# Performance work log

Measured on AMD Instinct MI355X. Metric: run time of the kernel, lower is better.

## Reference

```python
import jax, jax.numpy as jnp
import numpy as np

N_SUPPORT = 65536
N_QUERY = 65536
FEAT = 1024
EMBED = 512
WAYS = 256


def setup_inputs() -> dict:
    key = jax.random.key(0)
    k1, k2, k3, k4 = jax.random.split(key, 4)
    support_images = jax.random.normal(k1, (N_SUPPORT, FEAT), dtype=jnp.float32)
    query_images = jax.random.normal(k2, (N_QUERY, FEAT), dtype=jnp.float32)
    # deterministic labels so every one of the `ways` classes is non-empty
    labels = jnp.arange(N_SUPPORT, dtype=jnp.int32) % WAYS
    support_labels = jax.nn.one_hot(labels, WAYS, dtype=jnp.int32)  # one-hot, as in torch forward
    W = jax.random.normal(k3, (FEAT, EMBED), dtype=jnp.float32) / np.sqrt(FEAT).astype(np.float32)
    b = jax.random.normal(k4, (EMBED,), dtype=jnp.float32) * 0.01
    return {
        "support_images": support_images,
        "support_labels": support_labels,
        "query_images": query_images,
        "W": W,
        "b": b,
    }


def reference(support_images, support_labels, query_images, W, b):
    ways = support_labels.shape[1]
    labels = jnp.argmax(support_labels, axis=1)  # [N_support]

    # backbone: Linear(feat -> embed)
    z_support = support_images @ W + b  # [N_support, E]
    z_query = query_images @ W + b      # [N_query, E]

    # fused per-class mean (replaces the python loop over classes)
    sums = jax.ops.segment_sum(z_support, labels, num_segments=ways)          # [ways, E]
    counts = jax.ops.segment_sum(jnp.ones((z_support.shape[0],), z_support.dtype),
                                 labels, num_segments=ways)                   # [ways]
    z_proto = sums / counts[:, None]

    # scores = -cdist(z_query, z_proto)  (euclidean, p=2)
    q2 = jnp.sum(z_query * z_query, axis=1, keepdims=True)   # [Nq, 1]
    p2 = jnp.sum(z_proto * z_proto, axis=1)[None, :]          # [1, ways]
    d2 = q2 + p2 - 2.0 * (z_query @ z_proto.T)                # [Nq, ways]
    scores = -jnp.sqrt(jnp.maximum(d2, 0.0))

    return jax.nn.softmax(scores, axis=1)
```

## Files before the change

### kernel.cpp

```cpp
#include <hip/hip_runtime.h>
#include <stdint.h>

#define NSUP 65536
#define NQRY 65536
#define FEAT 1024
#define EMB  512
#define WAYS 256

typedef unsigned short u16;
typedef unsigned int   u32;
typedef __attribute__((ext_vector_type(8))) __bf16 bf16x8;
typedef __attribute__((ext_vector_type(4))) float  f32x4;

static __device__ __forceinline__ u16 f2bf(float f) {
    u32 u = __builtin_bit_cast(u32, f);
    u32 r = u + 0x7fffu + ((u >> 16) & 1u);
    return (u16)(r >> 16);
}

static __device__ __forceinline__ void gl_lds16(const void* g, void* l) {
    __builtin_amdgcn_global_load_lds((const __attribute__((address_space(1))) u32*)g,
                                     (__attribute__((address_space(3))) u32*)l,
                                     16, 0, 0);
}

__global__ __launch_bounds__(256) void k0_transpose(const float* __restrict__ W,
                                                    u16* __restrict__ Wt) {
    __shared__ float tile[64][65];
    const int bx = blockIdx.x;
    const int k0 = (bx & 15) * 64;
    const int e0 = (bx >> 4) * 64;
    const int t = threadIdx.x;
#pragma unroll
    for (int i = 0; i < 16; ++i) {
        int idx = t + i * 256;
        int kk = idx >> 6, ee = idx & 63;
        tile[kk][ee] = W[(size_t)(k0 + kk) * EMB + e0 + ee];
    }
    __syncthreads();
#pragma unroll
    for (int i = 0; i < 16; ++i) {
        int idx = t + i * 256;
        int ee = idx >> 6, kk = idx & 63;
        Wt[(size_t)(e0 + ee) * FEAT + k0 + kk] = f2bf(tile[kk][ee]);
    }
}

__global__ __launch_bounds__(256) void k1a_labels(const int* __restrict__ sl,
                                                  int* __restrict__ labels,
                                                  int* __restrict__ icounts) {
    const int row = blockIdx.x * 4 + (threadIdx.x >> 6);
    const int lane = threadIdx.x & 63;
    const int4* p = (const int4*)(sl + (size_t)row * WAYS);
    int4 v = p[lane];
    int my = -1;
    if (v.x) my = lane * 4 + 0;
    if (v.y) my = lane * 4 + 1;
    if (v.z) my = lane * 4 + 2;
    if (v.w) my = lane * 4 + 3;
#pragma unroll
    for (int m = 32; m; m >>= 1) my = max(my, __shfl_xor(my, m));
    if (lane == 0) {
        labels[row] = my;
        atomicAdd(&icounts[my], 1);
    }
}

__global__ __launch_bounds__(256) void k1p_prefix(const int* __restrict__ icounts,
                                                  int* __restrict__ offs,
                                                  int* __restrict__ cursor,
                                                  float* __restrict__ countsF) {
    __shared__ int s[256];
    const int t = threadIdx.x;
    const int v = icounts[t];
    s[t] = v;
    __syncthreads();
    for (int d = 1; d < 256; d <<= 1) {
        int x = (t >= d) ? s[t - d] : 0;
        __syncthreads();
        s[t] += x;
        __syncthreads();
    }
    const int exc = s[t] - v;
    offs[t] = exc;
    cursor[t] = exc;
    countsF[t] = (float)v;
}

__global__ __launch_bounds__(256) void k1s_scatter(const int* __restrict__ labels,
                                                   int* __restrict__ cursor,
                                                   int* __restrict__ perm) {
    const int r = blockIdx.x * 256 + threadIdx.x;
    const int lb = labels[r];
    const int pos = atomicAdd(&cursor[lb], 1);
    perm[pos] = r;
}

__global__ __launch_bounds__(256) void k1c_classsum(const float* __restrict__ img,
                                                    const int* __restrict__ perm,
                                                    const int* __restrict__ offs,
                                                    const int* __restrict__ icounts,
                                                    float* __restrict__ sums) {
    const int c  = blockIdx.x >> 2;
    const int fs = blockIdx.x & 3;
    const int t  = threadIdx.x;
    const int base = offs[c];
    const int n    = icounts[c];
    const size_t fcol = (size_t)fs * 256 + t;
    float acc = 0.f;
    int i = 0;
    for (; i + 8 <= n; i += 8) {
        int rr[8];
#pragma unroll
        for (int u = 0; u < 8; ++u) rr[u] = perm[base + i + u];
        float v[8];
#pragma unroll
        for (int u = 0; u < 8; ++u) v[u] = img[(size_t)rr[u] * FEAT + fcol];
#pragma unroll
        for (int u = 0; u < 8; ++u) acc += v[u];
    }
    for (; i < n; ++i) acc += img[(size_t)perm[base + i] * FEAT + fcol];
    sums[(size_t)c * FEAT + fcol] = acc;
}

__global__ __launch_bounds__(512) void k2_proto(const float* __restrict__ sums,
                                                const float* __restrict__ counts,
                                                const float* __restrict__ W,
                                                u16* __restrict__ zpb,
                                                float* __restrict__ p2) {
    __shared__ float proto[FEAT];
    __shared__ float red[8];
    const int c = blockIdx.x, t = threadIdx.x;
    const float inv = 1.0f / counts[c];
    proto[t]       = sums[(size_t)c * FEAT + t] * inv;
    proto[t + 512] = sums[(size_t)c * FEAT + t + 512] * inv;
    __syncthreads();
    float a0 = 0.f, a1 = 0.f, a2 = 0.f, a3 = 0.f;
#pragma unroll 8
    for (int k = 0; k < FEAT; k += 4) {
        a0 += proto[k + 0] * W[(size_t)(k + 0) * EMB + t];
        a1 += proto[k + 1] * W[(size_t)(k + 1) * EMB + t];
        a2 += proto[k + 2] * W[(size_t)(k + 2) * EMB + t];
        a3 += proto[k + 3] * W[(size_t)(k + 3) * EMB + t];
    }
    float z = (a0 + a1) + (a2 + a3);
    zpb[(size_t)c * EMB + t] = f2bf(z);
    float sq = z * z;
#pragma unroll
    for (int m = 1; m < 64; m <<= 1) sq += __shfl_xor(sq, m);
    if ((t & 63) == 0) red[t >> 6] = sq;
    __syncthreads();
    if (t == 0) {
        float s = 0.f;
#pragma unroll
        for (int i = 0; i < 8; ++i) s += red[i];
        p2[c] = s;
    }
}

__global__ __launch_bounds__(512, 2) void k3_zq(const float* __restrict__ Q,
                                                const u16* __restrict__ Wt,
                                                u16* __restrict__ zq,
                                                float* __restrict__ q2) {
    __shared__ u16 Asl[2][128 * 32];
    __shared__ u16 Bsl[2][512 * 32];
    __shared__ float q2l[128];
    const int t = threadIdx.x;
    const int lane = t & 63, wave = t >> 6;
    const int wm = wave >> 2, wn = wave & 3;
    const size_t row0 = (size_t)blockIdx.x * 128;

    if (t < 128) q2l[t] = 0.f;

    const int arow = t >> 2, aseg = t & 3;
    const float* aptr = Q + (row0 + arow) * FEAT + aseg * 8;
    u16* awr[2] = { &Asl[0][arow * 32 + aseg * 8], &Asl[1][arow * 32 + aseg * 8] };
    float af[8];

    auto loadA = [&](int ks) {
        const float4* p = (const float4*)(aptr + ks * 32);
        float4 x = p[0], y = p[1];
        af[0] = x.x; af[1] = x.y; af[2] = x.z; af[3] = x.w;
        af[4] = y.x; af[5] = y.y; af[6] = y.z; af[7] = y.w;
    };
    auto writeA = [&](int buf) {
        uint4 w;
        w.x = (u32)f2bf(af[0]) | ((u32)f2bf(af[1]) << 16);
        w.y = (u32)f2bf(af[2]) | ((u32)f2bf(af[3]) << 16);
        w.z = (u32)f2bf(af[4]) | ((u32)f2bf(af[5]) << 16);
        w.w = (u32)f2bf(af[6]) | ((u32)f2bf(af[7]) << 16);
        *(uint4*)awr[buf] = w;
    };
    auto stageB = [&](int buf, int ks) {
#pragma unroll
        for (int p = 0; p < 4; ++p) {
            int gi = t + p * 512;
            int n = gi >> 2, slot = gi & 3;
            gl_lds16(Wt + (size_t)n * FEAT + ks * 32 + slot * 8, &Bsl[buf][gi * 8]);
        }
    };

    f32x4 acc[4][8];
#pragma unroll
    for (int mt = 0; mt < 4; ++mt)
#pragma unroll
        for (int nt = 0; nt < 8; ++nt) acc[mt][nt] = f32x4{0.f, 0.f, 0.f, 0.f};

    stageB(0, 0);
    loadA(0);
    writeA(0);
    __syncthreads();

    const int ard = (wm * 64 + (lane & 15)) * 32 + (lane >> 4) * 8;
    const int brd = (wn * 128 + (lane & 15)) * 32 + (lane >> 4) * 8;

    int cur = 0;
    for (int ks = 0; ks < 32; ++ks) {
        const int nxt = cur ^ 1;
        if (ks < 31) { stageB(nxt, ks + 1); loadA(ks + 1); }
        bf16x8 a[4], b[8];
#pragma unroll
        for (int mt = 0; mt < 4; ++mt) a[mt] = *(const bf16x8*)&Asl[cur][ard + mt * 512];
#pragma unroll
        for (int nt = 0; nt < 8; ++nt) b[nt] = *(const bf16x8*)&Bsl[cur][brd + nt * 512];
#pragma unroll
        for (int mt = 0; mt < 4; ++mt)
#pragma unroll
            for (int nt = 0; nt < 8; ++nt)
                acc[mt][nt] = __builtin_amdgcn_mfma_f32_16x16x32_bf16(a[mt], b[nt], acc[mt][nt], 0, 0, 0);
        if (ks < 31) writeA(nxt);
        __syncthreads();
        cur = nxt;
    }

    const int g = lane >> 4, c = lane & 15;
#pragma unroll
    for (int mt = 0; mt < 4; ++mt) {
#pragma unroll
        for (int j = 0; j < 4; ++j) {
            const int rloc = wm * 64 + mt * 16 + g * 4 + j;
            const size_t r = row0 + rloc;
            float ss = 0.f;
#pragma unroll
            for (int nt = 0; nt < 8; ++nt) {
                float v = acc[mt][nt][j];
                ss += v * v;
                zq[r * EMB + wn * 128 + nt * 16 + c] = f2bf(v);
            }
#pragma unroll
            for (int m = 1; m < 16; m <<= 1) ss += __shfl_xor(ss, m);
            if (c == 0) atomicAdd(&q2l[rloc], ss);
        }
    }
    __syncthreads();
    if (t < 128) q2[row0 + t] = q2l[t];
}

__global__ __launch_bounds__(512, 2) void k4_scores(const u16* __restrict__ zq,
                                                    const u16* __restrict__ zp,
                                                    const float* __restrict__ q2,
                                                    const float* __restrict__ p2,
                                                    float* __restrict__ out) {
    __shared__ u16 Asl[2][128 * 32];
    __shared__ u16 Bsl[2][256 * 32];
    __shared__ float p2l[WAYS];
    const int t = threadIdx.x;
    const int lane = t & 63, wave = t >> 6;
    const size_t row0 = (size_t)blockIdx.x * 128;
    if (t < WAYS) p2l[t] = p2[t];

    auto stage = [&](int buf, int ks) {
        { int n = t >> 2, slot = t & 3;
          gl_lds16(zq + (row0 + n) * EMB + ks * 32 + slot * 8, &Asl[buf][t * 8]); }
#pragma unroll
        for (int p = 0; p < 2; ++p) {
            int gi = t + p * 512;
            int n = gi >> 2, slot = gi & 3;
            gl_lds16(zp + (size_t)n * EMB + ks * 32 + slot * 8, &Bsl[buf][gi * 8]);
        }
    };

    f32x4 acc[16];
#pragma unroll
    for (int nt = 0; nt < 16; ++nt) acc[nt] = f32x4{0.f, 0.f, 0.f, 0.f};

    stage(0, 0);
    __syncthreads();

    const int ard = (wave * 16 + (lane & 15)) * 32 + (lane >> 4) * 8;
    const int brd = (lane & 15) * 32 + (lane >> 4) * 8;

    int cur = 0;
    for (int ks = 0; ks < 16; ++ks) {
        const int nxt = cur ^ 1;
        if (ks < 15) stage(nxt, ks + 1);
        bf16x8 a = *(const bf16x8*)&Asl[cur][ard];
#pragma unroll
        for (int nt = 0; nt < 16; ++nt) {
            bf16x8 b = *(const bf16x8*)&Bsl[cur][brd + nt * 512];
            acc[nt] = __builtin_amdgcn_mfma_f32_16x16x32_bf16(a, b, acc[nt], 0, 0, 0);
        }
        __syncthreads();
        cur = nxt;
    }

    const int g = lane >> 4, c = lane & 15;
    float q2v[4], mx[4], sm[4];
#pragma unroll
    for (int j = 0; j < 4; ++j) {
        q2v[j] = q2[row0 + wave * 16 + g * 4 + j];
        mx[j] = -1e30f;
    }
#pragma unroll
    for (int nt = 0; nt < 16; ++nt) {
        float pp = p2l[nt * 16 + c];
#pragma unroll
        for (int j = 0; j < 4; ++j) {
            float d2 = q2v[j] + pp - 2.f * acc[nt][j];
            float s = -sqrtf(fmaxf(d2, 0.f));
            acc[nt][j] = s;
            mx[j] = fmaxf(mx[j], s);
        }
    }
#pragma unroll
    for (int j = 0; j < 4; ++j) {
#pragma unroll
        for (int m = 1; m < 16; m <<= 1) mx[j] = fmaxf(mx[j], __shfl_xor(mx[j], m));
        sm[j] = 0.f;
    }
#pragma unroll
    for (int nt = 0; nt < 16; ++nt)
#pragma unroll
        for (int j = 0; j < 4; ++j) {
            float e = __expf(acc[nt][j] - mx[j]);
            acc[nt][j] = e;
            sm[j] += e;
        }
#pragma unroll
    for (int j = 0; j < 4; ++j) {
#pragma unroll
        for (int m = 1; m < 16; m <<= 1) sm[j] += __shfl_xor(sm[j], m);
        sm[j] = 1.f / sm[j];
    }
#pragma unroll
    for (int nt = 0; nt < 16; ++nt)
#pragma unroll
        for (int j = 0; j < 4; ++j)
            out[(row0 + wave * 16 + g * 4 + j) * WAYS + nt * 16 + c] = acc[nt][j] * sm[j];
}

extern "C" void kernel_launch(void* const* d_in, const int* in_sizes, int n_in,
                              void* d_out, int out_size, void* d_ws, size_t ws_size,
                              hipStream_t stream) {
    (void)in_sizes; (void)n_in; (void)out_size; (void)ws_size;
    const float* simg = (const float*)d_in[0];
    const int*   slab = (const int*)d_in[1];
    const float* qimg = (const float*)d_in[2];
    const float* W    = (const float*)d_in[3];
    float* out = (float*)d_out;
    char* ws = (char*)d_ws;

    int*   labels = (int*)  (ws + 0);
    int*   perm   = (int*)  (ws + 262144);
    int*   icounts= (int*)  (ws + 524288);
    int*   offs   = (int*)  (ws + 525312);
    int*   cursor = (int*)  (ws + 526336);
    float* countsF= (float*)(ws + 527360);
    float* sums   = (float*)(ws + 528384);
    float* p2     = (float*)(ws + 1576960);
    u16*   zpb    = (u16*)  (ws + 1577984);
    u16*   Wt     = (u16*)  (ws + 1840128);
    u16*   zq     = (u16*)  (ws + 2888704);
    float* q2     = (float*)(ws + 69997568);

    hipMemsetAsync(icounts, 0, 1024, stream);

    k0_transpose <<<128,        256, 0, stream>>>(W, Wt);
    k1a_labels   <<<NSUP / 4,   256, 0, stream>>>(slab, labels, icounts);
    k1p_prefix   <<<1,          256, 0, stream>>>(icounts, offs, cursor, countsF);
    k1s_scatter  <<<NSUP / 256, 256, 0, stream>>>(labels, cursor, perm);
    k1c_classsum <<<WAYS * 4,   256, 0, stream>>>(simg, perm, offs, icounts, sums);
    k2_proto     <<<WAYS,       512, 0, stream>>>(sums, countsF, W, zpb, p2);
    k3_zq        <<<NQRY / 128, 512, 0, stream>>>(qimg, Wt, zq, q2);
    k4_scores    <<<NQRY / 128, 512, 0, stream>>>(zq, zpb, q2, p2, out);
}
```

Measured before the change: 378.5 us.

## Split query GEMM over N halves, swizzle LDS, retile score GEMM to 2x4 waves

k3_zq now splits each 128-row tile into two blocks covering 256 embedding columns each. This halves the per-block B tile and accumulators so launch bounds can allow 4 blocks per CU, and q2 is combined across the two blocks with a global atomicAdd after a memset. Both GEMM kernels use an XOR swizzle on the LDS layout to reduce bank conflicts. k4_scores uses a 2x4 wave tile, with the softmax max and sum reduced across waves through LDS. The cost is that k3 reads each query row twice (fp32 A loaded by both halves), plus extra syncs and atomics.

```diff
diff --git a/kernel.cpp b/kernel.cpp
--- a/kernel.cpp
+++ b/kernel.cpp
@@ -22,6 +22,10 @@
     __builtin_amdgcn_global_load_lds((const __attribute__((address_space(1))) u32*)g,
                                      (__attribute__((address_space(3))) u32*)l,
                                      16, 0, 0);
+}
+
+static __device__ __forceinline__ int swz16(int r, int s) {
+    return r * 32 + ((s ^ ((r >> 1) & 3)) * 8);
 }
 
 __global__ __launch_bounds__(256) void k0_transpose(const float* __restrict__ W,
@@ -158,23 +162,24 @@
     }
 }
 
-__global__ __launch_bounds__(512, 2) void k3_zq(const float* __restrict__ Q,
+__global__ __launch_bounds__(512, 4) void k3_zq(const float* __restrict__ Q,
                                                 const u16* __restrict__ Wt,
                                                 u16* __restrict__ zq,
                                                 float* __restrict__ q2) {
     __shared__ u16 Asl[2][128 * 32];
-    __shared__ u16 Bsl[2][512 * 32];
+    __shared__ u16 Bsl[2][256 * 32];
     __shared__ float q2l[128];
     const int t = threadIdx.x;
     const int lane = t & 63, wave = t >> 6;
     const int wm = wave >> 2, wn = wave & 3;
-    const size_t row0 = (size_t)blockIdx.x * 128;
+    const size_t row0 = (size_t)(blockIdx.x >> 1) * 128;
+    const int n0 = (blockIdx.x & 1) * 256;
 
     if (t < 128) q2l[t] = 0.f;
 
-    const int arow = t >> 2, aseg = t & 3;
-    const float* aptr = Q + (row0 + arow) * FEAT + aseg * 8;
-    u16* awr[2] = { &Asl[0][arow * 32 + aseg * 8], &Asl[1][arow * 32 + aseg * 8] };
+    const int ar = t >> 2, as = t & 3;
+    const float* aptr = Q + (row0 + ar) * FEAT + as * 8;
+    const int aw = swz16(ar, as);
     float af[8];
 
     auto loadA = [&](int ks) {
@@ -189,51 +194,53 @@
         w.y = (u32)f2bf(af[2]) | ((u32)f2bf(af[3]) << 16);
         w.z = (u32)f2bf(af[4]) | ((u32)f2bf(af[5]) << 16);
         w.w = (u32)f2bf(af[6]) | ((u32)f2bf(af[7]) << 16);
-        *(uint4*)awr[buf] = w;
+        *(uint4*)&Asl[buf][aw] = w;
     };
     auto stageB = [&](int buf, int ks) {
 #pragma unroll
-        for (int p = 0; p < 4; ++p) {
+        for (int p = 0; p < 2; ++p) {
             int gi = t + p * 512;
-            int n = gi >> 2, slot = gi & 3;
-            gl_lds16(Wt + (size_t)n * FEAT + ks * 32 + slot * 8, &Bsl[buf][gi * 8]);
+            int r = gi >> 2, cc = gi & 3;
+            int s = cc ^ ((r >> 1) & 3);
+            gl_lds16(Wt + (size_t)(n0 + r) * FEAT + ks * 32 + s * 8, &Bsl[buf][gi * 8]);
         }
     };
 
-    f32x4 acc[4][8];
+    f32x4 acc[4][4];
 #pragma unroll
     for (int mt = 0; mt < 4; ++mt)
 #pragma unroll
-        for (int nt = 0; nt < 8; ++nt) acc[mt][nt] = f32x4{0.f, 0.f, 0.f, 0.f};
+        for (int nt = 0; nt < 4; ++nt) acc[mt][nt] = f32x4{0.f, 0.f, 0.f, 0.f};
 
     stageB(0, 0);
     loadA(0);
     writeA(0);
     __syncthreads();
 
-    const int ard = (wm * 64 + (lane & 15)) * 32 + (lane >> 4) * 8;
-    const int brd = (wn * 128 + (lane & 15)) * 32 + (lane >> 4) * 8;
+    const int L = lane & 15, g = lane >> 4;
+    const int ard = swz16(wm * 64 + L, g);
+    const int brd = swz16(wn * 64 + L, g);
 
     int cur = 0;
     for (int ks = 0; ks < 32; ++ks) {
         const int nxt = cur ^ 1;
         if (ks < 31) { stageB(nxt, ks + 1); loadA(ks + 1); }
-        bf16x8 a[4], b[8];
+        bf16x8 a[4], b[4];
 #pragma unroll
         for (int mt = 0; mt < 4; ++mt) a[mt] = *(const bf16x8*)&Asl[cur][ard + mt * 512];
 #pragma unroll
-        for (int nt = 0; nt < 8; ++nt) b[nt] = *(const bf16x8*)&Bsl[cur][brd + nt * 512];
+        for (int nt = 0; nt < 4; ++nt) b[nt] = *(const bf16x8*)&Bsl[cur][brd + nt * 512];
 #pragma unroll
         for (int mt = 0; mt < 4; ++mt)
 #pragma unroll
-            for (int nt = 0; nt < 8; ++nt)
+            for (int nt = 0; nt < 4; ++nt)
                 acc[mt][nt] = __builtin_amdgcn_mfma_f32_16x16x32_bf16(a[mt], b[nt], acc[mt][nt], 0, 0, 0);
         if (ks < 31) writeA(nxt);
         __syncthreads();
         cur = nxt;
     }
 
-    const int g = lane >> 4, c = lane & 15;
+    const int c = L;
 #pragma unroll
     for (int mt = 0; mt < 4; ++mt) {
 #pragma unroll
@@ -242,10 +249,10 @@
             const size_t r = row0 + rloc;
             float ss = 0.f;
 #pragma unroll
-            for (int nt = 0; nt < 8; ++nt) {
+            for (int nt = 0; nt < 4; ++nt) {
                 float v = acc[mt][nt][j];
                 ss += v * v;
-                zq[r * EMB + wn * 128 + nt * 16 + c] = f2bf(v);
+                zq[r * EMB + n0 + wn * 64 + nt * 16 + c] = f2bf(v);
             }
 #pragma unroll
             for (int m = 1; m < 16; m <<= 1) ss += __shfl_xor(ss, m);
@@ -253,10 +260,10 @@
         }
     }
     __syncthreads();
-    if (t < 128) q2[row0 + t] = q2l[t];
-}
-
-__global__ __launch_bounds__(512, 2) void k4_scores(const u16* __restrict__ zq,
+    if (t < 128) atomicAdd(&q2[row0 + t], q2l[t]);
+}
+
+__global__ __launch_bounds__(512, 4) void k4_scores(const u16* __restrict__ zq,
                                                     const u16* __restrict__ zp,
                                                     const float* __restrict__ q2,
                                                     const float* __restrict__ p2,
@@ -264,89 +271,111 @@
     __shared__ u16 Asl[2][128 * 32];
     __shared__ u16 Bsl[2][256 * 32];
     __shared__ float p2l[WAYS];
+    __shared__ float q2s[128];
     const int t = threadIdx.x;
     const int lane = t & 63, wave = t >> 6;
+    const int wm = wave >> 2, wn = wave & 3;
     const size_t row0 = (size_t)blockIdx.x * 128;
     if (t < WAYS) p2l[t] = p2[t];
+    if (t >= WAYS && t < WAYS + 128) q2s[t - WAYS] = q2[row0 + t - WAYS];
 
     auto stage = [&](int buf, int ks) {
-        { int n = t >> 2, slot = t & 3;
-          gl_lds16(zq + (row0 + n) * EMB + ks * 32 + slot * 8, &Asl[buf][t * 8]); }
+        { int r = t >> 2, cc = t & 3;
+          int s = cc ^ ((r >> 1) & 3);
+          gl_lds16(zq + (row0 + r) * EMB + ks * 32 + s * 8, &Asl[buf][t * 8]); }
 #pragma unroll
         for (int p = 0; p < 2; ++p) {
             int gi = t + p * 512;
-            int n = gi >> 2, slot = gi & 3;
-            gl_lds16(zp + (size_t)n * EMB + ks * 32 + slot * 8, &Bsl[buf][gi * 8]);
+            int r = gi >> 2, cc = gi & 3;
+            int s = cc ^ ((r >> 1) & 3);
+            gl_lds16(zp + (size_t)r * EMB + ks * 32 + s * 8, &Bsl[buf][gi * 8]);
         }
     };
 
-    f32x4 acc[16];
-#pragma unroll
-    for (int nt = 0; nt < 16; ++nt) acc[nt] = f32x4{0.f, 0.f, 0.f, 0.f};
+    f32x4 acc[4][4];
+#pragma unroll
+    for (int mt = 0; mt < 4; ++mt)
+#pragma unroll
+        for (int nt = 0; nt < 4; ++nt) acc[mt][nt] = f32x4{0.f, 0.f, 0.f, 0.f};
 
     stage(0, 0);
     __syncthreads();
 
-    const int ard = (wave * 16 + (lane & 15)) * 32 + (lane >> 4) * 8;
-    const int brd = (lane & 15) * 32 + (lane >> 4) * 8;
+    const int L = lane & 15, g = lane >> 4;
+    const int ard = swz16(wm * 64 + L, g);
+    const int brd = swz16(wn * 64 + L, g);
 
     int cur = 0;
     for (int ks = 0; ks < 16; ++ks) {
         const int nxt = cur ^ 1;
         if (ks < 15) stage(nxt, ks + 1);
-        bf16x8 a = *(const bf16x8*)&Asl[cur][ard];
-#pragma unroll
-        for (int nt = 0; nt < 16; ++nt) {
-            bf16x8 b = *(const bf16x8*)&Bsl[cur][brd + nt * 512];
-            acc[nt] = __builtin_amdgcn_mfma_f32_16x16x32_bf16(a, b, acc[nt], 0, 0, 0);
-        }
+        bf16x8 a[4], b[4];
+#pragma unroll
+        for (int mt = 0; mt < 4; ++mt) a[mt] = *(const bf16x8*)&Asl[cur][ard + mt * 512];
+#pragma unroll
+        for (int nt = 0; nt < 4; ++nt) b[nt] = *(const bf16x8*)&Bsl[cur][brd + nt * 512];
+#pragma unroll
+        for (int mt = 0; mt < 4; ++mt)
+#pragma unroll
+            for (int nt = 0; nt < 4; ++nt)
+                acc[mt][nt] = __builtin_amdgcn_mfma_f32_16x16x32_bf16(a[mt], b[nt], acc[mt][nt], 0, 0, 0);
         __syncthreads();
         cur = nxt;
     }
 
-    const int g = lane >> 4, c = lane & 15;
-    float q2v[4], mx[4], sm[4];
-#pragma unroll
-    for (int j = 0; j < 4; ++j) {
-        q2v[j] = q2[row0 + wave * 16 + g * 4 + j];
-        mx[j] = -1e30f;
-    }
-#pragma unroll
-    for (int nt = 0; nt < 16; ++nt) {
-        float pp = p2l[nt * 16 + c];
+    float* rmax = (float*)&Asl[0][0];
+    float* rsum = rmax + 512;
+    const int c = L;
+
+#pragma unroll
+    for (int mt = 0; mt < 4; ++mt)
 #pragma unroll
         for (int j = 0; j < 4; ++j) {
-            float d2 = q2v[j] + pp - 2.f * acc[nt][j];
-            float s = -sqrtf(fmaxf(d2, 0.f));
-            acc[nt][j] = s;
-            mx[j] = fmaxf(mx[j], s);
-        }
-    }
-#pragma unroll
-    for (int j = 0; j < 4; ++j) {
-#pragma unroll
-        for (int m = 1; m < 16; m <<= 1) mx[j] = fmaxf(mx[j], __shfl_xor(mx[j], m));
-        sm[j] = 0.f;
-    }
-#pragma unroll
-    for (int nt = 0; nt < 16; ++nt)
+            const int rloc = wm * 64 + mt * 16 + g * 4 + j;
+            const float qv = q2s[rloc];
+            float m_ = -1e30f;
+#pragma unroll
+            for (int nt = 0; nt < 4; ++nt) {
+                float d2 = qv + p2l[wn * 64 + nt * 16 + c] - 2.f * acc[mt][nt][j];
+                float s = -sqrtf(fmaxf(d2, 0.f));
+                acc[mt][nt][j] = s;
+                m_ = fmaxf(m_, s);
+            }
+#pragma unroll
+            for (int m = 1; m < 16; m <<= 1) m_ = fmaxf(m_, __shfl_xor(m_, m));
+            if (c == 0) rmax[rloc * 4 + wn] = m_;
+        }
+    __syncthreads();
+#pragma unroll
+    for (int mt = 0; mt < 4; ++mt)
 #pragma unroll
         for (int j = 0; j < 4; ++j) {
-            float e = __expf(acc[nt][j] - mx[j]);
-            acc[nt][j] = e;
-            sm[j] += e;
-        }
-#pragma unroll
-    for (int j = 0; j < 4; ++j) {
-#pragma unroll
-        for (int m = 1; m < 16; m <<= 1) sm[j] += __shfl_xor(sm[j], m);
-        sm[j] = 1.f / sm[j];
-    }
-#pragma unroll
-    for (int nt = 0; nt < 16; ++nt)
-#pragma unroll
-        for (int j = 0; j < 4; ++j)
-            out[(row0 + wave * 16 + g * 4 + j) * WAYS + nt * 16 + c] = acc[nt][j] * sm[j];
+            const int rloc = wm * 64 + mt * 16 + g * 4 + j;
+            float m4 = fmaxf(fmaxf(rmax[rloc * 4 + 0], rmax[rloc * 4 + 1]),
+                             fmaxf(rmax[rloc * 4 + 2], rmax[rloc * 4 + 3]));
+            float s_ = 0.f;
+#pragma unroll
+            for (int nt = 0; nt < 4; ++nt) {
+                float e = __expf(acc[mt][nt][j] - m4);
+                acc[mt][nt][j] = e;
+                s_ += e;
+            }
+#pragma unroll
+            for (int m = 1; m < 16; m <<= 1) s_ += __shfl_xor(s_, m);
+            if (c == 0) rsum[rloc * 4 + wn] = s_;
+        }
+    __syncthreads();
+#pragma unroll
+    for (int mt = 0; mt < 4; ++mt)
+#pragma unroll
+        for (int j = 0; j < 4; ++j) {
+            const int rloc = wm * 64 + mt * 16 + g * 4 + j;
+            float inv = 1.f / ((rsum[rloc * 4 + 0] + rsum[rloc * 4 + 1]) +
+                               (rsum[rloc * 4 + 2] + rsum[rloc * 4 + 3]));
+#pragma unroll
+            for (int nt = 0; nt < 4; ++nt)
+                out[(row0 + rloc) * WAYS + wn * 64 + nt * 16 + c] = acc[mt][nt][j] * inv;
+        }
 }
 
 extern "C" void kernel_launch(void* const* d_in, const int* in_sizes, int n_in,
@@ -374,13 +403,14 @@
     float* q2     = (float*)(ws + 69997568);
 
     hipMemsetAsync(icounts, 0, 1024, stream);
-
-    k0_transpose <<<128,        256, 0, stream>>>(W, Wt);
-    k1a_labels   <<<NSUP / 4,   256, 0, stream>>>(slab, labels, icounts);
-    k1p_prefix   <<<1,          256, 0, stream>>>(icounts, offs, cursor, countsF);
-    k1s_scatter  <<<NSUP / 256, 256, 0, stream>>>(labels, cursor, perm);
-    k1c_classsum <<<WAYS * 4,   256, 0, stream>>>(simg, perm, offs, icounts, sums);
-    k2_proto     <<<WAYS,       512, 0, stream>>>(sums, countsF, W, zpb, p2);
-    k3_zq        <<<NQRY / 128, 512, 0, stream>>>(qimg, Wt, zq, q2);
-    k4_scores    <<<NQRY / 128, 512, 0, stream>>>(zq, zpb, q2, p2, out);
-}
+    hipMemsetAsync(q2, 0, 262144, stream);
+
+    k0_transpose <<<128,            256, 0, stream>>>(W, Wt);
+    k1a_labels   <<<NSUP / 4,       256, 0, stream>>>(slab, labels, icounts);
+    k1p_prefix   <<<1,              256, 0, stream>>>(icounts, offs, cursor, countsF);
+    k1s_scatter  <<<NSUP / 256,     256, 0, stream>>>(labels, cursor, perm);
+    k1c_classsum <<<WAYS * 4,       256, 0, stream>>>(simg, perm, offs, icounts, sums);
+    k2_proto     <<<WAYS,           512, 0, stream>>>(sums, countsF, W, zpb, p2);
+    k3_zq        <<<(NQRY/128) * 2, 512, 0, stream>>>(qimg, Wt, zq, q2);
+    k4_scores    <<<NQRY / 128,     512, 0, stream>>>(zq, zpb, q2, p2, out);
+}
```

New measurement: 378.7 us. No clear change (+0.1%).
